# Performance work log

Hardware: AMD Instinct MI355X
Metric: run time of the kernel (lower is better)

## Reference

```python
import jax, jax.numpy as jnp
import numpy as np


def setup_inputs() -> dict:
    key = jax.random.key(0)
    k1, k2, k3, k4, k5 = jax.random.split(key, 5)
    B, S, T = 32, 2048, 512
    return {
        "unary_potentials": jax.random.normal(k1, (B, S, T), dtype=jnp.float32),
        "binary_potentials": jax.random.normal(k2, (T, T), dtype=jnp.float32),
        "tags": jax.random.randint(k3, (B, S), 0, T, dtype=jnp.int32),
        "predicted_tags": jax.random.randint(k4, (B, S), 0, T, dtype=jnp.int32),
        "mask": jax.random.randint(k5, (B, S), 0, 2, dtype=jnp.int32),
    }


def _score(unary, binary, tags, mask):
    # unary: [B,S,T], binary: [T,T], tags/mask: [B,S]
    B, S, T = unary.shape
    seq_len = jnp.sum(mask, axis=-1)              # [B]; original iterates range(sum(mask))
    pos = jnp.arange(S)
    valid = (pos[None, :] < seq_len[:, None]).astype(unary.dtype)      # [B,S]
    # unary score: unary[b, i, tags[b, i]] for i < seq_len
    un = jnp.take_along_axis(unary, tags[..., None], axis=2)[..., 0]   # [B,S]
    # transition score: binary[tags[b, i-1], tags[b, i]] for 1 <= i < seq_len
    tr = binary[tags[:, :-1], tags[:, 1:]]                             # [B,S-1]
    valid_tr = (pos[1:][None, :] < seq_len[:, None]).astype(unary.dtype)
    return jnp.sum(un * valid, axis=-1) + jnp.sum(tr * valid_tr, axis=-1)  # [B]


def reference(unary_potentials, binary_potentials, tags, predicted_tags, mask):
    gold = _score(unary_potentials, binary_potentials, tags, mask)
    pred = _score(unary_potentials, binary_potentials, predicted_tags, mask)
    losses = jnp.maximum(pred - gold, 0.0)
    return jnp.sum(losses)
```

## Files before the change

kernel.cpp:

```cpp
#include <hip/hip_runtime.h>


#define BB 32
#define SS 2048
#define TT 512

__global__ __launch_bounds__(256) void sp_batch_kernel(
    const float* __restrict__ unary,
    const float* __restrict__ binary,
    const int*   __restrict__ tags,
    const int*   __restrict__ pred,
    const int*   __restrict__ mask,
    float*       __restrict__ ws)
{
    const int b   = blockIdx.x;
    const int tid = threadIdx.x;
    const int wave = tid >> 6;

    __shared__ int   s_ipart[4];
    __shared__ float s_part[8];
    __shared__ int   s_len;

    int m = 0;
    for (int s = tid; s < SS; s += 256) m += mask[b * SS + s];
    #pragma unroll
    for (int off = 32; off > 0; off >>= 1) m += __shfl_down(m, off);
    if ((tid & 63) == 0) s_ipart[wave] = m;
    __syncthreads();
    if (tid == 0) s_len = s_ipart[0] + s_ipart[1] + s_ipart[2] + s_ipart[3];
    __syncthreads();
    const int L = s_len;

    float g = 0.f, p = 0.f;
    for (int s = tid; s < SS; s += 256) {
        if (s < L) {
            const int base = b * SS + s;
            const int tg = tags[base];
            const int tp = pred[base];
            g += unary[base * TT + tg];
            p += unary[base * TT + tp];
            if (s >= 1) {
                const int tg0 = tags[base - 1];
                const int tp0 = pred[base - 1];
                g += binary[tg0 * TT + tg];
                p += binary[tp0 * TT + tp];
            }
        }
    }
    #pragma unroll
    for (int off = 32; off > 0; off >>= 1) {
        g += __shfl_down(g, off);
        p += __shfl_down(p, off);
    }
    if ((tid & 63) == 0) { s_part[wave * 2] = g; s_part[wave * 2 + 1] = p; }
    __syncthreads();
    if (tid == 0) {
        const float G = s_part[0] + s_part[2] + s_part[4] + s_part[6];
        const float P = s_part[1] + s_part[3] + s_part[5] + s_part[7];
        ws[b] = fmaxf(P - G, 0.f);
    }
}

__global__ __launch_bounds__(64) void sp_final_kernel(
    const float* __restrict__ ws, float* __restrict__ out)
{
    const int tid = threadIdx.x;
    float v = (tid < BB) ? ws[tid] : 0.f;
    #pragma unroll
    for (int off = 32; off > 0; off >>= 1) v += __shfl_down(v, off);
    if (tid == 0) out[0] = v;
}

extern "C" void kernel_launch(void* const* d_in, const int* in_sizes, int n_in,
                              void* d_out, int out_size, void* d_ws, size_t ws_size,
                              hipStream_t stream) {
    const float* unary  = (const float*)d_in[0];
    const float* binary = (const float*)d_in[1];
    const int*   tags   = (const int*)d_in[2];
    const int*   pred   = (const int*)d_in[3];
    const int*   mask   = (const int*)d_in[4];
    float* ws  = (float*)d_ws;
    float* out = (float*)d_out;

    sp_batch_kernel<<<BB, 256, 0, stream>>>(unary, binary, tags, pred, mask, ws);
    sp_final_kernel<<<1, 64, 0, stream>>>(ws, out);
}
```

Before: 12.55 us.

## Issue gathers before mask reduction and fuse final sum via atomicAdd

Loads all eight unary and binary gathers per thread into registers up front, overlapping them with the mask sum instead of waiting for the sequence length first, then applies the length mask when accumulating. The separate final-reduction kernel is replaced by a memset plus an atomicAdd from each block. This removes a serial dependency and a kernel launch, at the cost of doing gathers for positions past the sequence length and making the float summation order nondeterministic.

```diff
diff --git a/kernel.cpp b/kernel.cpp
--- a/kernel.cpp
+++ b/kernel.cpp
@@ -5,16 +5,16 @@
 #define SS 2048
 #define TT 512
 
-__global__ __launch_bounds__(256) void sp_batch_kernel(
+__global__ __launch_bounds__(256) void sp_fused_kernel(
     const float* __restrict__ unary,
     const float* __restrict__ binary,
     const int*   __restrict__ tags,
     const int*   __restrict__ pred,
     const int*   __restrict__ mask,
-    float*       __restrict__ ws)
+    float*       __restrict__ out)
 {
-    const int b   = blockIdx.x;
-    const int tid = threadIdx.x;
+    const int b    = blockIdx.x;
+    const int tid  = threadIdx.x;
     const int wave = tid >> 6;
 
     __shared__ int   s_ipart[4];
@@ -22,7 +22,26 @@
     __shared__ int   s_len;
 
     int m = 0;
-    for (int s = tid; s < SS; s += 256) m += mask[b * SS + s];
+    float vg[8], vp[8];
+    #pragma unroll
+    for (int k = 0; k < 8; ++k) {
+        const int s    = tid + k * 256;
+        const int base = b * SS + s;
+        const int tg = tags[base];
+        const int tp = pred[base];
+        m += mask[base];
+        float g = unary[base * TT + tg];
+        float p = unary[base * TT + tp];
+        if (s >= 1) {
+            const int tg0 = tags[base - 1];
+            const int tp0 = pred[base - 1];
+            g += binary[tg0 * TT + tg];
+            p += binary[tp0 * TT + tp];
+        }
+        vg[k] = g;
+        vp[k] = p;
+    }
+
     #pragma unroll
     for (int off = 32; off > 0; off >>= 1) m += __shfl_down(m, off);
     if ((tid & 63) == 0) s_ipart[wave] = m;
@@ -32,20 +51,10 @@
     const int L = s_len;
 
     float g = 0.f, p = 0.f;
-    for (int s = tid; s < SS; s += 256) {
-        if (s < L) {
-            const int base = b * SS + s;
-            const int tg = tags[base];
-            const int tp = pred[base];
-            g += unary[base * TT + tg];
-            p += unary[base * TT + tp];
-            if (s >= 1) {
-                const int tg0 = tags[base - 1];
-                const int tp0 = pred[base - 1];
-                g += binary[tg0 * TT + tg];
-                p += binary[tp0 * TT + tp];
-            }
-        }
+    #pragma unroll
+    for (int k = 0; k < 8; ++k) {
+        const int s = tid + k * 256;
+        if (s < L) { g += vg[k]; p += vp[k]; }
     }
     #pragma unroll
     for (int off = 32; off > 0; off >>= 1) {
@@ -57,18 +66,8 @@
     if (tid == 0) {
         const float G = s_part[0] + s_part[2] + s_part[4] + s_part[6];
         const float P = s_part[1] + s_part[3] + s_part[5] + s_part[7];
-        ws[b] = fmaxf(P - G, 0.f);
+        atomicAdd(out, fmaxf(P - G, 0.f));
     }
-}
-
-__global__ __launch_bounds__(64) void sp_final_kernel(
-    const float* __restrict__ ws, float* __restrict__ out)
-{
-    const int tid = threadIdx.x;
-    float v = (tid < BB) ? ws[tid] : 0.f;
-    #pragma unroll
-    for (int off = 32; off > 0; off >>= 1) v += __shfl_down(v, off);
-    if (tid == 0) out[0] = v;
 }
 
 extern "C" void kernel_launch(void* const* d_in, const int* in_sizes, int n_in,
@@ -79,9 +78,8 @@
     const int*   tags   = (const int*)d_in[2];
     const int*   pred   = (const int*)d_in[3];
     const int*   mask   = (const int*)d_in[4];
-    float* ws  = (float*)d_ws;
     float* out = (float*)d_out;
 
-    sp_batch_kernel<<<BB, 256, 0, stream>>>(unary, binary, tags, pred, mask, ws);
-    sp_final_kernel<<<1, 64, 0, stream>>>(ws, out);
+    hipMemsetAsync(out, 0, sizeof(float), stream);
+    sp_fused_kernel<<<BB, 256, 0, stream>>>(unary, binary, tags, pred, mask, out);
 }
```

Measured after the change: 20.21 us. 61.0% more time.
